# Kernel tuning notes

Hardware: AMD Instinct MI355X
Metric: run time of the kernel (lower is better)

Reference implementation:

```python
import jax, jax.numpy as jnp
import numpy as np
from jax import lax

# NOTE: ResidualConvBlock and SS2DChanelFirst are reconstructed from the repo's
# conventions: ResidualConvBlock = act(conv3x3 -> act -> conv3x3 + 1x1 skip);
# SS2DChanelFirst = standard VMamba SS2D (in_proj -> dw-conv3x3 -> SiLU ->
# 4-direction cross-scan selective scan -> cross-merge -> LayerNorm -> *SiLU(z)
# gate -> out_proj) operating on NCHW tensors.

B, CIN, H, W = 4, 6, 64, 64
DM, DI, K, N, R, NL, GROUPS = 72, 144, 4, 8, 4, 2, 12


def conv2d(x, w, b=None, groups=1):
    out = lax.conv_general_dilated(x, w, (1, 1), 'SAME',
                                   dimension_numbers=('NCHW', 'OIHW', 'NCHW'),
                                   feature_group_count=groups)
    if b is not None:
        out = out + b[None, :, None, None]
    return out


def lrelu(x, s):
    return jnp.where(x >= 0, x, s * x)


def selective_scan(u, delta, A, Bs, Cs, D):
    # u, delta: (b,K,C,L); A: (K,C,N); Bs, Cs: (b,K,N,L); D: (K,C)
    b, k, c, l = u.shape
    n = A.shape[-1]
    ul = jnp.moveaxis(u, -1, 0)
    dl = jnp.moveaxis(delta, -1, 0)
    Bl = jnp.moveaxis(Bs, -1, 0)
    Cl = jnp.moveaxis(Cs, -1, 0)
    h0 = jnp.zeros((b, k, c, n), u.dtype)

    def step(h, xt):
        d_t, u_t, B_t, C_t = xt
        h = h * jnp.exp(d_t[..., None] * A) + (d_t * u_t)[..., None] * B_t[:, :, None, :]
        return h, jnp.einsum('bkcn,bkn->bkc', h, C_t)

    _, ys = lax.scan(step, h0, (dl, ul, Bl, Cl))
    return jnp.moveaxis(ys, 0, -1) + u * D[None, :, :, None]


def ss2d(x, in_w, dw_w, dw_b, xp_w, dtp_w, dtp_b, A_logs, Ds, ong, onb, op_w):
    b, dm, h_, w_ = x.shape
    l = h_ * w_
    xz = jnp.einsum('ec,bchw->behw', in_w, x)  # (b, 2*DI, h, w)
    xi, z = xz[:, :DI], xz[:, DI:]
    xi = jax.nn.silu(conv2d(xi, dw_w, dw_b, groups=DI))
    # cross-scan: row-major, col-major, and their reverses
    x0 = xi.reshape(b, DI, l)
    x1 = jnp.swapaxes(xi, 2, 3).reshape(b, DI, l)
    xs = jnp.stack([x0, x1, x0[..., ::-1], x1[..., ::-1]], axis=1)  # (b,4,DI,l)
    x_dbl = jnp.einsum('bkdl,kcd->bkcl', xs, xp_w)  # (b,4,R+2N,l)
    dts, Bs, Cs = x_dbl[:, :, :R], x_dbl[:, :, R:R + N], x_dbl[:, :, R + N:]
    dts = jnp.einsum('bkrl,kdr->bkdl', dts, dtp_w)
    delta = jax.nn.softplus(dts + dtp_b[None, :, :, None])
    A = -jnp.exp(A_logs).reshape(K, DI, N)
    ys = selective_scan(xs, delta, A, Bs, Cs, Ds.reshape(K, DI))  # (b,4,DI,l)
    # cross-merge
    y = ys[:, 0] + ys[:, 2, :, ::-1]
    yt = ys[:, 1] + ys[:, 3, :, ::-1]
    y = y + jnp.swapaxes(yt.reshape(b, DI, w_, h_), 2, 3).reshape(b, DI, l)
    y = jnp.swapaxes(y, 1, 2)  # (b,l,DI)
    mu = y.mean(-1, keepdims=True)
    var = ((y - mu) ** 2).mean(-1, keepdims=True)
    y = (y - mu) / jnp.sqrt(var + 1e-5) * ong + onb
    y = y * jax.nn.silu(jnp.swapaxes(z.reshape(b, DI, l), 1, 2))
    out = jnp.einsum('bld,ed->ble', y, op_w)  # (b,l,DM)
    return jnp.swapaxes(out, 1, 2).reshape(b, dm, h_, w_)


def groupnorm(x, g, bta, groups):
    b, c, h_, w_ = x.shape
    xg = x.reshape(b, groups, c // groups, h_ * w_)
    mu = xg.mean((2, 3), keepdims=True)
    var = ((xg - mu) ** 2).mean((2, 3), keepdims=True)
    xg = (xg - mu) / jnp.sqrt(var + 1e-5)
    return xg.reshape(b, c, h_, w_) * g[None, :, None, None] + bta[None, :, None, None]


def setup_inputs() -> dict:
    key = jax.random.key(0)
    ks = iter(jax.random.split(key, 32))
    nrm = lambda shp, s=0.05: jax.random.normal(next(ks), shp, jnp.float32) * s
    inp = {
        'image': jax.random.normal(next(ks), (B, CIN, H, W), jnp.float32),
        'cb_w1': nrm((DM, CIN, 3, 3), 0.1), 'cb_b1': nrm((DM,), 0.02),
        'cb_w2': nrm((DM, DM, 3, 3), 0.05), 'cb_b2': nrm((DM,), 0.02),
        'cb_ws': nrm((DM, CIN, 1, 1), 0.1), 'cb_bs': nrm((DM,), 0.02),
        'in_w': nrm((NL, 2 * DI, DM), 0.05),
        'dw_w': nrm((NL, DI, 1, 3, 3), 0.1), 'dw_b': nrm((NL, DI), 0.02),
        'xp_w': nrm((NL, K, R + 2 * N, DI), 0.05),
        'dtp_w': nrm((NL, K, DI, R), 0.1), 'dtp_b': nrm((NL, K, DI), 0.1),
        'A_logs': nrm((NL, K * DI, N), 0.5),
        'Ds': jnp.ones((NL, K * DI), jnp.float32) + nrm((NL, K * DI), 0.05),
        'ong': jnp.ones((NL, DI), jnp.float32), 'onb': jnp.zeros((NL, DI), jnp.float32),
        'op_w': nrm((NL, DM, DI), 0.05),
        'gn_g': jnp.ones((NL, DM), jnp.float32), 'gn_b': jnp.zeros((NL, DM), jnp.float32),
        'l1_w': nrm((NL, DM, DM), 0.1), 'l1_b': nrm((NL, DM), 0.02),
        'l2_w': nrm((NL, DM, DM), 0.1), 'l2_b': nrm((NL, DM), 0.02),
        'shrink_w': nrm((CIN, DM, 3, 3), 0.05), 'shrink_b': nrm((CIN,), 0.02),
    }
    return inp


def reference(image, cb_w1, cb_b1, cb_w2, cb_b2, cb_ws, cb_bs, in_w, dw_w, dw_b,
              xp_w, dtp_w, dtp_b, A_logs, Ds, ong, onb, op_w, gn_g, gn_b,
              l1_w, l1_b, l2_w, l2_b, shrink_w, shrink_b):
    # ResidualConvBlock (expand 6 -> 72), leaky_relu
    h = lrelu(conv2d(image, cb_w1, cb_b1), 0.01)
    h = conv2d(h, cb_w2, cb_b2) + conv2d(image, cb_ws, cb_bs)
    x = lrelu(h, 0.01)
    for i in range(NL):
        x = ss2d(x, in_w[i], dw_w[i], dw_b[i], xp_w[i], dtp_w[i], dtp_b[i],
                 A_logs[i], Ds[i], ong[i], onb[i], op_w[i])
        x = groupnorm(x, gn_g[i], gn_b[i], GROUPS)
        x = jnp.einsum('oc,bchw->bohw', l1_w[i], x) + l1_b[i][None, :, None, None]
        x = lrelu(x, 0.04)
        x = jnp.einsum('oc,bchw->bohw', l2_w[i], x) + l2_b[i][None, :, None, None]
    x = conv2d(x, shrink_w, shrink_b)
    return jax.nn.sigmoid(x)
```

## Files before the change

### kernel.cpp

```cpp
#include <hip/hip_runtime.h>
#include <math.h>

#define BB 4
#define CI 6
#define LL 4096
#define DMC 72
#define DIC 144
#define KD 4
#define NS 8
#define RD 4
#define NLAYER 2
#define GRP 12
#define NCH 256
#define TS 16
#define SP 72
#define PPN (66*SP)
#define L2E 1.4426950408889634f

__device__ __forceinline__ float sigmoidf_(float x){ return 1.f/(1.f+__expf(-x)); }
__device__ __forceinline__ float siluf_(float x){ return x*sigmoidf_(x); }
__device__ __forceinline__ float softplusf_(float x){
  return fmaxf(x,0.f) + __logf(1.f + __expf(-fabsf(x)));
}

__device__ __forceinline__ int padidx(int p){ return SP*(p>>6) + (p&63) + SP + 4; }

#define LOAD9(ip, a) do { \
  a[0]=(ip)[-SP-1]; a[1]=(ip)[-SP]; a[2]=(ip)[-SP+1]; \
  a[3]=(ip)[-1];    a[4]=(ip)[0];   a[5]=(ip)[1];     \
  a[6]=(ip)[SP-1];  a[7]=(ip)[SP];  a[8]=(ip)[SP+1];  } while(0)

__device__ __forceinline__ void load6(const float* __restrict__ base, float v[6]){
  v[0] = base[-1];
  float4 f = *(const float4*)base;
  v[1]=f.x; v[2]=f.y; v[3]=f.z; v[4]=f.w;
  v[5] = base[4];
}

__global__ void k_halo(float* __restrict__ pads, int nplanes){
  int plane = blockIdx.x;
  if (plane >= nplanes) return;
  int t = threadIdx.x;
  if (t >= 260) return;
  float* pl = pads + (size_t)plane*PPN;
  int row, col;
  if (t < 132){
    row = (t < 66) ? 0 : 65;
    col = 3 + (t % 66);
  } else {
    int j = t - 132;
    col = (j < 64) ? 3 : 68;
    row = 1 + (j & 63);
  }
  pl[row*SP + col] = 0.f;
}

__global__ void k_pad_img(const float* __restrict__ img, float* __restrict__ img_pad){
  int idx = blockIdx.x*256 + threadIdx.x;
  if (idx >= BB*CI*LL) return;
  int p = idx & 4095; int bc = idx >> 12;
  img_pad[(size_t)bc*PPN + padidx(p)] = img[idx];
}

__global__ void k_conv1(const float* __restrict__ img_pad, const float* __restrict__ w,
                        const float* __restrict__ bias, float* __restrict__ tmp_pad){
  int bid = blockIdx.x;
  int tile = bid & 3; int r = bid >> 2; int o = r % DMC; int b = r / DMC;
  int p0 = tile*1024 + threadIdx.x*4;
  int pb = padidx(p0);
  float bv = bias[o];
  float acc[4] = {bv,bv,bv,bv};
  #pragma unroll
  for (int ic=0; ic<CI; ++ic){
    const float* ip = img_pad + (size_t)(b*CI+ic)*PPN + pb;
    const float* wr = w + (o*CI+ic)*9;
    #pragma unroll
    for (int rr=0; rr<3; ++rr){
      float v[6]; load6(ip + (rr-1)*SP, v);
      float w0=wr[rr*3], w1=wr[rr*3+1], w2v=wr[rr*3+2];
      #pragma unroll
      for (int q=0;q<4;++q) acc[q] += v[q]*w0 + v[q+1]*w1 + v[q+2]*w2v;
    }
  }
  #pragma unroll
  for (int q=0;q<4;++q) acc[q] = acc[q] >= 0.f ? acc[q] : 0.01f*acc[q];
  *(float4*)(tmp_pad + (size_t)(b*DMC+o)*PPN + pb) = make_float4(acc[0],acc[1],acc[2],acc[3]);
}

__global__ void k_conv2init(const float* __restrict__ img, const float* __restrict__ b2,
                            const float* __restrict__ wsc, const float* __restrict__ bsc,
                            float* __restrict__ xout){
  int bid = blockIdx.x;
  int t = bid & 15; int r = bid >> 4; int og = r % 18; int b = r / 18;
  int p = t*256 + threadIdx.x;
  float acc[4];
  #pragma unroll
  for (int j=0;j<4;++j) acc[j] = b2[og*4+j] + bsc[og*4+j];
  #pragma unroll
  for (int ic=0; ic<CI; ++ic){
    float v = img[((b*CI+ic)<<12)+p];
    #pragma unroll
    for (int j=0;j<4;++j) acc[j] += v * wsc[(og*4+j)*CI+ic];
  }
  #pragma unroll
  for (int j=0;j<4;++j)
    xout[((b*DMC+og*4+j)<<12)+p] = acc[j];
}

__global__ void k_conv2(const float* __restrict__ tmp_pad,
                        const float* __restrict__ w2, float* __restrict__ xout){
  int bid = blockIdx.x;
  int t = bid & 15; int r = bid >> 4; int og = r % 18; r /= 18;
  int icg = r & 1; int b = r >> 1;
  int p = t*256 + threadIdx.x;
  int pb = padidx(p);
  float acc[4] = {0.f,0.f,0.f,0.f};
  const float* ipb = tmp_pad + (size_t)b*DMC*PPN + pb;
  const float* wb  = w2 + (size_t)(og*4)*DMC*9;
  #pragma unroll 2
  for (int ii=0; ii<36; ++ii){
    int ic = icg*36 + ii;
    const float* ip = ipb + (size_t)ic*PPN;
    float a[9]; LOAD9(ip, a);
    const float* wp = wb + ic*9;
    #pragma unroll
    for (int j=0;j<4;++j){
      float s = 0.f;
      #pragma unroll
      for (int q=0;q<9;++q) s += a[q]*wp[(size_t)j*DMC*9 + q];
      acc[j] += s;
    }
  }
  #pragma unroll
  for (int j=0;j<4;++j)
    atomicAdd(xout + ((b*DMC+og*4+j)<<12)+p, acc[j]);
}

__global__ void k_xz(const float* __restrict__ x, const float* __restrict__ inw,
                     float* __restrict__ xz_pad, float* __restrict__ z_t, int relu){
  int bid = blockIdx.x;
  int t = bid & 15; int r = bid >> 4; int eg = r % 36; int b = r / 36;
  int p = t*256 + threadIdx.x;
  float acc[8] = {0.f,0.f,0.f,0.f,0.f,0.f,0.f,0.f};
  for (int c0=0; c0<DMC; c0+=4){
    float a[4];
    #pragma unroll
    for (int q=0;q<4;++q) a[q] = x[((b*DMC+c0+q)<<12)+p];
    if (relu){
      #pragma unroll
      for (int q=0;q<4;++q) a[q] = a[q] >= 0.f ? a[q] : 0.01f*a[q];
    }
    #pragma unroll
    for (int j=0;j<8;++j){
      float4 w = *(const float4*)(inw + (eg*8+j)*DMC + c0);
      acc[j] += a[0]*w.x + a[1]*w.y + a[2]*w.z + a[3]*w.w;
    }
  }
  if (eg < 18){
    int pb = padidx(p);
    #pragma unroll
    for (int j=0;j<8;++j) xz_pad[(size_t)(b*DIC+eg*8+j)*PPN + pb] = acc[j];
  } else {
    float* zb = z_t + ((size_t)b*LL+p)*DIC + (eg*8-DIC);
    *(float4*)(zb)   = make_float4(acc[0],acc[1],acc[2],acc[3]);
    *(float4*)(zb+4) = make_float4(acc[4],acc[5],acc[6],acc[7]);
  }
}

__global__ void k_dw(const float* __restrict__ xz_pad, const float* __restrict__ dww,
                     const float* __restrict__ dwb, float* __restrict__ xi_t){
  int bid = blockIdx.x;
  int tile = bid & 3; int r = bid >> 2; int c = r % DIC; int b = r / DIC;
  int p0 = tile*1024 + threadIdx.x*4;
  int pb = padidx(p0);
  const float* ip = xz_pad + (size_t)(b*DIC+c)*PPN + pb;
  const float* wp = dww + c*9;
  float bv = dwb[c];
  float acc[4] = {bv,bv,bv,bv};
  #pragma unroll
  for (int rr=0; rr<3; ++rr){
    float v[6]; load6(ip + (rr-1)*SP, v);
    float w0=wp[rr*3], w1=wp[rr*3+1], w2v=wp[rr*3+2];
    #pragma unroll
    for (int q=0;q<4;++q) acc[q] += v[q]*w0 + v[q+1]*w1 + v[q+2]*w2v;
  }
  #pragma unroll
  for (int q=0;q<4;++q)
    xi_t[((size_t)b*LL+p0+q)*DIC + c] = siluf_(acc[q]);
}

__global__ void k_xdbl(const float* __restrict__ xi_t, const float* __restrict__ xpw,
                       float* __restrict__ xdbl){
  int bid = blockIdx.x;
  int t = bid & 15; int r = bid >> 4;
  int kk = r & 3; r >>= 2; int part = r & 3; int b = r >> 2;
  int p = t*256 + threadIdx.x;
  const float* xib = xi_t + ((size_t)b*LL + p)*DIC;
  const float* wk = xpw + (size_t)(kk*20 + part*5)*DIC;
  float acc[5] = {0.f,0.f,0.f,0.f,0.f};
  for (int d=0; d<DIC; d+=4){
    float4 v = *(const float4*)(xib + d);
    #pragma unroll
    for (int c=0;c<5;++c){
      float4 w = *(const float4*)(wk + (size_t)c*DIC + d);
      acc[c] += v.x*w.x + v.y*w.y + v.z*w.z + v.w*w.w;
    }
  }
  float* dst = xdbl + ((size_t)(b*KD+kk)*LL + p)*20 + part*5;
  #pragma unroll
  for (int c=0;c<5;++c) dst[c] = acc[c];
}

__device__ __forceinline__ void scan_decode(int idx, int& b, int& k, int& ch, int& c){
  c = idx % DIC;
  int r = idx / DIC;
  ch = r % NCH;
  r /= NCH;
  k = r & 3; b = r >> 2;
}

__device__ __forceinline__ void scan_affine(int k, int ch, int& ps0, int& sk){
  int l0 = ch*TS;
  if (k == 0){ ps0 = l0; sk = 1; }
  else if (k == 1){ ps0 = ((l0 & 63) << 6) | (l0 >> 6); sk = 64; }
  else if (k == 2){ ps0 = (LL-1) - l0; sk = -1; }
  else { int m0 = (LL-1) - l0; ps0 = ((m0 & 63) << 6) | (m0 >> 6); sk = -64; }
}

__global__ void k_p1(const float* __restrict__ xi_t, const float* __restrict__ xdbl,
                     const float* __restrict__ dtpw, const float* __restrict__ dtpb,
                     const float* __restrict__ alog,
                     float* __restrict__ cumA, float* __restrict__ hp){
  int idx = blockIdx.x*256 + threadIdx.x;
  if (idx >= BB*KD*NCH*DIC) return;
  int b,k,ch,c; scan_decode(idx,b,k,ch,c);
  float Arow[NS];
  #pragma unroll
  for (int n=0;n<NS;++n) Arow[n] = -__expf(alog[(k*DIC+c)*NS+n]) * L2E;
  float4 wdt = *(const float4*)(dtpw + (k*DIC+c)*RD);
  float bdt = dtpb[k*DIC+c];
  int ps0, sk; scan_affine(k, ch, ps0, sk);
  const float* row = xdbl + (size_t)(b*KD+k)*LL*20 + (size_t)ps0*20;
  const float* up  = xi_t + (size_t)b*LL*DIC + c + (size_t)ps0*DIC;
  long rstep = (long)sk*20;
  long ustep = (long)sk*DIC;
  float h[NS];
  #pragma unroll
  for (int n=0;n<NS;++n) h[n]=0.f;
  float sumd = 0.f;
  #pragma unroll 4
  for (int t=0; t<TS; ++t){
    float4 q0 = *(const float4*)(row);
    float4 q1 = *(const float4*)(row+4);
    float4 q2 = *(const float4*)(row+8);
    float u = *up;
    float dt = bdt + q0.x*wdt.x + q0.y*wdt.y + q0.z*wdt.z + q0.w*wdt.w;
    dt = softplusf_(dt);
    sumd += dt;
    float du = dt*u;
    float Bv[NS] = {q1.x,q1.y,q1.z,q1.w,q2.x,q2.y,q2.z,q2.w};
    #pragma unroll
    for (int n=0;n<NS;++n)
      h[n] = h[n]*exp2f(dt*Arow[n]) + du*Bv[n];
    row += rstep; up += ustep;
  }
  size_t base = ((size_t)((b*KD+k)*NCH + ch)*NS)*DIC + c;
  #pragma unroll
  for (int n=0;n<NS;++n) hp[base + n*DIC] = h[n];
  #pragma unroll
  for (int n=0;n<NS;++n) cumA[base + n*DIC] = exp2f(sumd*Arow[n]);
}

__global__ void k_p2(float* __restrict__ cumA, float* __restrict__ hp,
                     float* __restrict__ gnstats){
  if (blockIdx.x == 0 && threadIdx.x < 2*BB*GRP) gnstats[threadIdx.x] = 0.f;
  int idx = blockIdx.x*256 + threadIdx.x;
  if (idx >= BB*KD*NS*DIC) return;
  int c = idx % DIC; int n = (idx/DIC) % NS; int bk = idx/(DIC*NS);
  float h = 0.f;
  #pragma unroll 8
  for (int ch=0; ch<NCH; ++ch){
    size_t base = ((size_t)(bk*NCH+ch)*NS + n)*DIC + c;
    float a = cumA[base];
    float pp = hp[base];
    cumA[base] = 0.f;
    hp[base] = h;
    h = a*h + pp;
  }
}

__global__ void k_p3(const float* __restrict__ xi_t, const float* __restrict__ xdbl,
                     const float* __restrict__ dtpw, const float* __restrict__ dtpb,
                     const float* __restrict__ alog, const float* __restrict__ Dsv,
                     const float* __restrict__ hin, float* __restrict__ y_t){
  int idx = blockIdx.x*256 + threadIdx.x;
  if (idx >= BB*KD*NCH*DIC) return;
  int b,k,ch,c; scan_decode(idx,b,k,ch,c);
  float Arow[NS];
  #pragma unroll
  for (int n=0;n<NS;++n) Arow[n] = -__expf(alog[(k*DIC+c)*NS+n]) * L2E;
  float4 wdt = *(const float4*)(dtpw + (k*DIC+c)*RD);
  float bdt = dtpb[k*DIC+c];
  float Dv = Dsv[k*DIC+c];
  int ps0, sk; scan_affine(k, ch, ps0, sk);
  const float* row = xdbl + (size_t)(b*KD+k)*LL*20 + (size_t)ps0*20;
  const float* up  = xi_t + (size_t)b*LL*DIC + c + (size_t)ps0*DIC;
  float* yp        = y_t  + (size_t)b*LL*DIC + c + (size_t)ps0*DIC;
  long rstep = (long)sk*20;
  long ustep = (long)sk*DIC;
  float h[NS];
  size_t base = ((size_t)((b*KD+k)*NCH + ch)*NS)*DIC + c;
  #pragma unroll
  for (int n=0;n<NS;++n) h[n] = hin[base + n*DIC];
  #pragma unroll 4
  for (int t=0; t<TS; ++t){
    float4 q0 = *(const float4*)(row);
    float4 q1 = *(const float4*)(row+4);
    float4 q2 = *(const float4*)(row+8);
    float4 q3 = *(const float4*)(row+12);
    float4 q4 = *(const float4*)(row+16);
    float u = *up;
    float dt = bdt + q0.x*wdt.x + q0.y*wdt.y + q0.z*wdt.z + q0.w*wdt.w;
    dt = softplusf_(dt);
    float du = dt*u;
    float Bv[NS] = {q1.x,q1.y,q1.z,q1.w,q2.x,q2.y,q2.z,q2.w};
    float Cv[NS] = {q3.x,q3.y,q3.z,q3.w,q4.x,q4.y,q4.z,q4.w};
    float y = 0.f;
    #pragma unroll
    for (int n=0;n<NS;++n){
      h[n] = h[n]*exp2f(dt*Arow[n]) + du*Bv[n];
      y += h[n]*Cv[n];
    }
    y += u*Dv;
    atomicAdd(yp, y);
    row += rstep; up += ustep; yp += ustep;
  }
}

__global__ void k_lnz(float* __restrict__ y_t, const float* __restrict__ z_t,
                      const float* __restrict__ ong, const float* __restrict__ onb){
  int gid = blockIdx.x*256 + threadIdx.x;
  int wid = gid >> 6;
  int lane = gid & 63;
  if (wid >= BB*LL) return;
  size_t rb = (size_t)wid * DIC;
  float v0 = y_t[rb + lane];
  float v1 = y_t[rb + 64 + lane];
  float v2 = (lane < 16) ? y_t[rb + 128 + lane] : 0.f;
  float s = v0 + v1 + v2;
  float q = v0*v0 + v1*v1 + v2*v2;
  #pragma unroll
  for (int o=32; o>0; o>>=1){ s += __shfl_xor(s,o,64); q += __shfl_xor(q,o,64); }
  float mu = s*(1.f/DIC);
  float var = q*(1.f/DIC) - mu*mu;
  float rs = rsqrtf(var + 1e-5f);
  float z0 = z_t[rb + lane];
  y_t[rb + lane] = ((v0-mu)*rs*ong[lane] + onb[lane]) * siluf_(z0);
  float z1 = z_t[rb + 64 + lane];
  y_t[rb + 64 + lane] = ((v1-mu)*rs*ong[64+lane] + onb[64+lane]) * siluf_(z1);
  if (lane < 16){
    float z2 = z_t[rb + 128 + lane];
    y_t[rb + 128 + lane] = ((v2-mu)*rs*ong[128+lane] + onb[128+lane]) * siluf_(z2);
  }
}

__global__ void k_oproj(const float* __restrict__ yn, const float* __restrict__ opw,
                        float* __restrict__ xout, float* __restrict__ gnstats){
  int bid = blockIdx.x;
  int t = bid & 15; int r = bid >> 4; int og = r % 18; int b = r / 18;
  int p = t*256 + threadIdx.x;
  const float* yb = yn + ((size_t)b*LL + p)*DIC;
  float acc[4] = {0.f,0.f,0.f,0.f};
  for (int d=0; d<DIC; d+=4){
    float4 v = *(const float4*)(yb + d);
    #pragma unroll
    for (int j=0;j<4;++j){
      float4 w = *(const float4*)(opw + (og*4+j)*DIC + d);
      acc[j] += v.x*w.x + v.y*w.y + v.z*w.z + v.w*w.w;
    }
  }
  #pragma unroll
  for (int j=0;j<4;++j)
    xout[((size_t)(b*DMC+og*4+j)<<12)+p] = acc[j];
  int c0 = og*4;
  int gA = c0/6;
  int nA = 6 - (c0 - gA*6);
  float sA=0.f,qA=0.f,sB=0.f,qB=0.f;
  #pragma unroll
  for (int j=0;j<4;++j){
    float v = acc[j];
    if (j < nA){ sA += v; qA += v*v; } else { sB += v; qB += v*v; }
  }
  #pragma unroll
  for (int o=32; o>0; o>>=1){
    sA += __shfl_xor(sA,o,64); qA += __shfl_xor(qA,o,64);
    sB += __shfl_xor(sB,o,64); qB += __shfl_xor(qB,o,64);
  }
  if ((threadIdx.x & 63) == 0){
    atomicAdd(gnstats + (b*GRP+gA)*2,     sA);
    atomicAdd(gnstats + (b*GRP+gA)*2 + 1, qA);
    if (nA < 4){
      atomicAdd(gnstats + (b*GRP+gA+1)*2,     sB);
      atomicAdd(gnstats + (b*GRP+gA+1)*2 + 1, qB);
    }
  }
}

__global__ void k_dense1(const float* __restrict__ xin, const float* __restrict__ gnstats,
                         const float* __restrict__ gng, const float* __restrict__ gnb,
                         const float* __restrict__ w, const float* __restrict__ bias,
                         float* __restrict__ xout){
  __shared__ float As[DMC], Bs[DMC];
  int bid = blockIdx.x;
  int t = bid & 15; int r = bid >> 4; int eg = r % 18; int b = r / 18;
  if (threadIdx.x < DMC){
    int c = threadIdx.x; int gr = c/6;
    float s = gnstats[(b*GRP+gr)*2];
    float q = gnstats[(b*GRP+gr)*2 + 1];
    const float inv = 1.f/(6.f*LL);
    float mu = s*inv;
    float var = q*inv - mu*mu;
    float rs = rsqrtf(var + 1e-5f);
    float A = rs*gng[c];
    As[c] = A;
    Bs[c] = gnb[c] - mu*A;
  }
  __syncthreads();
  int p = t*256 + threadIdx.x;
  float acc[4];
  #pragma unroll
  for (int j=0;j<4;++j) acc[j] = bias[eg*4+j];
  for (int c0=0; c0<DMC; c0+=4){
    float a[4];
    #pragma unroll
    for (int q=0;q<4;++q){
      float v = xin[((size_t)(b*DMC+c0+q)<<12)+p];
      a[q] = v*As[c0+q] + Bs[c0+q];
    }
    #pragma unroll
    for (int j=0;j<4;++j){
      float4 w0 = *(const float4*)(w + (eg*4+j)*DMC + c0);
      acc[j] += a[0]*w0.x + a[1]*w0.y + a[2]*w0.z + a[3]*w0.w;
    }
  }
  #pragma unroll
  for (int j=0;j<4;++j)
    xout[((size_t)(b*DMC+eg*4+j)<<12)+p] = acc[j];
}

__global__ void k_dense2(const float* __restrict__ xin, const float* __restrict__ w,
                         const float* __restrict__ bias, float* __restrict__ xout,
                         float* __restrict__ pad_out){
  int bid = blockIdx.x;
  int t = bid & 15; int r = bid >> 4; int eg = r % 18; int b = r / 18;
  int p = t*256 + threadIdx.x;
  float acc[4];
  #pragma unroll
  for (int j=0;j<4;++j) acc[j] = bias[eg*4+j];
  for (int c0=0; c0<DMC; c0+=4){
    float a[4];
    #pragma unroll
    for (int q=0;q<4;++q){
      float v = xin[((size_t)(b*DMC+c0+q)<<12)+p];
      a[q] = v >= 0.f ? v : 0.04f*v;
    }
    #pragma unroll
    for (int j=0;j<4;++j){
      float4 w0 = *(const float4*)(w + (eg*4+j)*DMC + c0);
      acc[j] += a[0]*w0.x + a[1]*w0.y + a[2]*w0.z + a[3]*w0.w;
    }
  }
  int pb = padidx(p);
  #pragma unroll
  for (int j=0;j<4;++j){
    xout[((size_t)(b*DMC+eg*4+j)<<12)+p] = acc[j];
    if (pad_out) pad_out[(size_t)(b*DMC+eg*4+j)*PPN + pb] = acc[j];
  }
}

__global__ void k_shrinkA(const float* __restrict__ x_pad, const float* __restrict__ w,
                          float* __restrict__ pacc){
  int bid = blockIdx.x;
  int t = bid & 15; int r = bid >> 4; int icg = r % 24; int b = r / 24;
  int p = t*256 + threadIdx.x;
  int pb = padidx(p);
  float acc[6] = {0.f,0.f,0.f,0.f,0.f,0.f};
  const float* ipb = x_pad + (size_t)b*DMC*PPN + pb;
  #pragma unroll
  for (int ii=0; ii<3; ++ii){
    int ic = icg*3 + ii;
    const float* ip = ipb + (size_t)ic*PPN;
    float a[9]; LOAD9(ip, a);
    #pragma unroll
    for (int o=0;o<6;++o){
      const float* wp = w + (o*DMC+ic)*9;
      float s = 0.f;
      #pragma unroll
      for (int q=0;q<9;++q) s += a[q]*wp[q];
      acc[o] += s;
    }
  }
  #pragma unroll
  for (int o=0;o<6;++o)
    atomicAdd(pacc + ((size_t)(b*CI+o)<<12)+p, acc[o]);
}

__global__ void k_sig(const float* __restrict__ pacc, const float* __restrict__ bias,
                      float* __restrict__ out){
  int idx = blockIdx.x*256 + threadIdx.x;
  if (idx >= BB*CI*LL) return;
  int o = (idx>>12) % CI;
  out[idx] = sigmoidf_(pacc[idx] + bias[o]);
}

extern "C" void kernel_launch(void* const* d_in, const int* in_sizes, int n_in,
                              void* d_out, int out_size, void* d_ws, size_t ws_size,
                              hipStream_t stream){
  const float* image = (const float*)d_in[0];
  const float* cb_w1 = (const float*)d_in[1];
  const float* cb_b1 = (const float*)d_in[2];
  const float* cb_w2 = (const float*)d_in[3];
  const float* cb_b2 = (const float*)d_in[4];
  const float* cb_ws = (const float*)d_in[5];
  const float* cb_bs = (const float*)d_in[6];
  const float* in_w  = (const float*)d_in[7];
  const float* dw_w  = (const float*)d_in[8];
  const float* dw_b  = (const float*)d_in[9];
  const float* xp_w  = (const float*)d_in[10];
  const float* dtp_w = (const float*)d_in[11];
  const float* dtp_b = (const float*)d_in[12];
  const float* A_logs= (const float*)d_in[13];
  const float* Ds    = (const float*)d_in[14];
  const float* ong   = (const float*)d_in[15];
  const float* onb   = (const float*)d_in[16];
  const float* op_w  = (const float*)d_in[17];
  const float* gn_g  = (const float*)d_in[18];
  const float* gn_b  = (const float*)d_in[19];
  const float* l1_w  = (const float*)d_in[20];
  const float* l1_b  = (const float*)d_in[21];
  const float* l2_w  = (const float*)d_in[22];
  const float* l2_b  = (const float*)d_in[23];
  const float* sh_w  = (const float*)d_in[24];
  const float* sh_b  = (const float*)d_in[25];

  const size_t SZ_X  = (size_t)BB*DMC*LL;
  const size_t SZ_C  = (size_t)BB*DIC*LL;
  const size_t SZ_XD = (size_t)BB*KD*20*LL;
  const size_t SZ_HP = (size_t)BB*KD*NCH*NS*DIC;
  const size_t SZ_IP = (size_t)BB*CI*PPN;
  const size_t SZ_TP = (size_t)BB*DMC*PPN;
  const size_t SZ_ZP = (size_t)BB*DIC*PPN;

  float* ws = (float*)d_ws;
  size_t off = 0;
  float* x     = ws + off; off += SZ_X;
  float* tmp   = ws + off; off += SZ_X;
  float* z_t   = ws + off; off += SZ_C;
  float* xi_t  = ws + off; off += SZ_C;
  float* xdbl  = ws + off; off += SZ_XD;
  float* cumA  = ws + off; off += SZ_HP;
  float* hp    = ws + off; off += SZ_HP;
  float* pads  = ws + off;
  float* img_pad = pads;
  float* tmp_pad = img_pad + SZ_IP;
  float* xz_pad  = tmp_pad + SZ_TP;
  off += SZ_IP + SZ_TP + SZ_ZP;
  float* gnstats = ws + off; off += 2*BB*GRP;
  if (ws_size < off*sizeof(float)) return;
  float* y_t = cumA;

  dim3 blk(256);
  const int NPLANES = BB*CI + BB*DMC + BB*DIC;

  k_halo<<<dim3(NPLANES), blk, 0, stream>>>(pads, NPLANES);
  k_pad_img<<<dim3(BB*CI*16), blk, 0, stream>>>(image, img_pad);
  k_conv1<<<dim3(BB*DMC*4), blk, 0, stream>>>(img_pad, cb_w1, cb_b1, tmp_pad);
  k_conv2init<<<dim3(BB*18*16), blk, 0, stream>>>(image, cb_b2, cb_ws, cb_bs, x);
  k_conv2<<<dim3(BB*2*18*16), blk, 0, stream>>>(tmp_pad, cb_w2, x);

  for (int i=0; i<NLAYER; ++i){
    const float* in_w_i  = in_w  + (size_t)i*2*DIC*DMC;
    const float* dw_w_i  = dw_w  + (size_t)i*DIC*9;
    const float* dw_b_i  = dw_b  + (size_t)i*DIC;
    const float* xp_w_i  = xp_w  + (size_t)i*KD*20*DIC;
    const float* dtp_w_i = dtp_w + (size_t)i*KD*DIC*RD;
    const float* dtp_b_i = dtp_b + (size_t)i*KD*DIC;
    const float* alog_i  = A_logs+ (size_t)i*KD*DIC*NS;
    const float* Ds_i    = Ds    + (size_t)i*KD*DIC;
    const float* ong_i   = ong   + (size_t)i*DIC;
    const float* onb_i   = onb   + (size_t)i*DIC;
    const float* op_w_i  = op_w  + (size_t)i*DMC*DIC;
    const float* gn_g_i  = gn_g  + (size_t)i*DMC;
    const float* gn_b_i  = gn_b  + (size_t)i*DMC;
    const float* l1_w_i  = l1_w  + (size_t)i*DMC*DMC;
    const float* l1_b_i  = l1_b  + (size_t)i*DMC;
    const float* l2_w_i  = l2_w  + (size_t)i*DMC*DMC;
    const float* l2_b_i  = l2_b  + (size_t)i*DMC;

    k_xz  <<<dim3(BB*36*16), blk, 0, stream>>>(x, in_w_i, xz_pad, z_t, (i==0)?1:0);
    k_dw  <<<dim3(BB*DIC*4), blk, 0, stream>>>(xz_pad, dw_w_i, dw_b_i, xi_t);
    k_xdbl<<<dim3(BB*4*KD*16), blk, 0, stream>>>(xi_t, xp_w_i, xdbl);
    k_p1  <<<dim3(BB*KD*NCH*DIC/256), blk, 0, stream>>>(xi_t, xdbl, dtp_w_i, dtp_b_i, alog_i, cumA, hp);
    k_p2  <<<dim3(BB*KD*NS*DIC/256), blk, 0, stream>>>(cumA, hp, gnstats);
    k_p3  <<<dim3(BB*KD*NCH*DIC/256), blk, 0, stream>>>(xi_t, xdbl, dtp_w_i, dtp_b_i, alog_i, Ds_i, hp, y_t);
    k_lnz <<<dim3(BB*LL/4), blk, 0, stream>>>(y_t, z_t, ong_i, onb_i);
    k_oproj<<<dim3(BB*18*16), blk, 0, stream>>>(y_t, op_w_i, x, gnstats);
    k_dense1<<<dim3(BB*18*16), blk, 0, stream>>>(x, gnstats, gn_g_i, gn_b_i, l1_w_i, l1_b_i, tmp);
    k_dense2<<<dim3(BB*18*16), blk, 0, stream>>>(tmp, l2_w_i, l2_b_i, x,
                                                 (i==NLAYER-1) ? tmp_pad : (float*)nullptr);
  }

  hipMemsetAsync(tmp, 0, (size_t)BB*CI*LL*sizeof(float), stream);
  k_shrinkA<<<dim3(BB*24*16), blk, 0, stream>>>(tmp_pad, sh_w, tmp);
  k_sig<<<dim3((BB*CI*LL+255)/256), blk, 0, stream>>>(tmp, sh_b, (float*)d_out);
}
```

Baseline: 592.7 us.

## Tile out-projection through shared memory and split GroupNorm stats into own kernel

The out-projection now stages a 64-pixel by 72-channel slice of the normalized activations transposed in shared memory, and each wave computes 9 output channels. Each block handles half of the input channels and adds its partial sums into the output with atomics, so the LayerNorm kernel now zeroes the output buffer first. GroupNorm statistics move out of the projection into a separate reduction kernel that rereads the output. The aim is to reuse each activation load across more outputs and raise per-thread work, at the cost of global atomics, one extra kernel launch, and an extra pass over the output.

```diff
diff --git a/kernel.cpp b/kernel.cpp
--- a/kernel.cpp
+++ b/kernel.cpp
@@ -338,8 +338,11 @@
 }
 
 __global__ void k_lnz(float* __restrict__ y_t, const float* __restrict__ z_t,
-                      const float* __restrict__ ong, const float* __restrict__ onb){
+                      const float* __restrict__ ong, const float* __restrict__ onb,
+                      float* __restrict__ xzero){
   int gid = blockIdx.x*256 + threadIdx.x;
+  xzero[gid] = 0.f;
+  if (gid < (int)(BB*DMC*LL - BB*LL*64)) xzero[gid + BB*LL*64] = 0.f;
   int wid = gid >> 6;
   int lane = gid & 63;
   if (wid >= BB*LL) return;
@@ -365,44 +368,55 @@
 }
 
 __global__ void k_oproj(const float* __restrict__ yn, const float* __restrict__ opw,
-                        float* __restrict__ xout, float* __restrict__ gnstats){
-  int bid = blockIdx.x;
-  int t = bid & 15; int r = bid >> 4; int og = r % 18; int b = r / 18;
-  int p = t*256 + threadIdx.x;
-  const float* yb = yn + ((size_t)b*LL + p)*DIC;
-  float acc[4] = {0.f,0.f,0.f,0.f};
-  for (int d=0; d<DIC; d+=4){
-    float4 v = *(const float4*)(yb + d);
-    #pragma unroll
-    for (int j=0;j<4;++j){
-      float4 w = *(const float4*)(opw + (og*4+j)*DIC + d);
-      acc[j] += v.x*w.x + v.y*w.y + v.z*w.z + v.w*w.w;
-    }
-  }
-  #pragma unroll
-  for (int j=0;j<4;++j)
-    xout[((size_t)(b*DMC+og*4+j)<<12)+p] = acc[j];
-  int c0 = og*4;
-  int gA = c0/6;
-  int nA = 6 - (c0 - gA*6);
-  float sA=0.f,qA=0.f,sB=0.f,qB=0.f;
-  #pragma unroll
-  for (int j=0;j<4;++j){
-    float v = acc[j];
-    if (j < nA){ sA += v; qA += v*v; } else { sB += v; qB += v*v; }
-  }
-  #pragma unroll
-  for (int o=32; o>0; o>>=1){
-    sA += __shfl_xor(sA,o,64); qA += __shfl_xor(qA,o,64);
-    sB += __shfl_xor(sB,o,64); qB += __shfl_xor(qB,o,64);
-  }
-  if ((threadIdx.x & 63) == 0){
-    atomicAdd(gnstats + (b*GRP+gA)*2,     sA);
-    atomicAdd(gnstats + (b*GRP+gA)*2 + 1, qA);
-    if (nA < 4){
-      atomicAdd(gnstats + (b*GRP+gA+1)*2,     sB);
-      atomicAdd(gnstats + (b*GRP+gA+1)*2 + 1, qB);
-    }
+                        float* __restrict__ xout){
+  __shared__ float ly[72*65];
+  int bid = blockIdx.x;
+  int dhalf = bid & 1; int r = bid >> 1;
+  int tile = r & 63; int b = r >> 6;
+  int pstart = tile*64;
+  const float* src = yn + ((size_t)b*LL + pstart)*DIC + dhalf*72;
+  for (int i = threadIdx.x; i < 64*72; i += 512){
+    int px = i / 72; int d = i - px*72;
+    ly[d*65 + px] = src[(size_t)px*DIC + d];
+  }
+  __syncthreads();
+  int px = threadIdx.x & 63;
+  int ocg = __builtin_amdgcn_readfirstlane(threadIdx.x >> 6);
+  float acc[9];
+  #pragma unroll
+  for (int j=0;j<9;++j) acc[j]=0.f;
+  const float* wb = opw + (size_t)ocg*9*DIC + dhalf*72;
+  #pragma unroll 4
+  for (int d=0; d<72; ++d){
+    float a = ly[d*65 + px];
+    #pragma unroll
+    for (int j=0;j<9;++j) acc[j] += a * wb[(size_t)j*DIC + d];
+  }
+  #pragma unroll
+  for (int j=0;j<9;++j)
+    atomicAdd(xout + ((size_t)(b*DMC + ocg*9 + j)<<12) + pstart + px, acc[j]);
+}
+
+__global__ void k_gnA(const float* __restrict__ x, float* __restrict__ stats){
+  __shared__ float s1[256], s2[256];
+  int bid = blockIdx.x;
+  int t = bid & 15; int r = bid >> 4; int gr = r % GRP; int b = r / GRP;
+  float ls=0.f, lq=0.f;
+  #pragma unroll
+  for (int it=0; it<6; ++it){
+    int i = t*1536 + it*256 + threadIdx.x;
+    int c = gr*6 + (i>>12); int p = i & 4095;
+    float v = x[((size_t)(b*DMC+c)<<12)+p];
+    ls += v; lq += v*v;
+  }
+  s1[threadIdx.x]=ls; s2[threadIdx.x]=lq; __syncthreads();
+  for (int s=128; s>0; s>>=1){
+    if (threadIdx.x < s){ s1[threadIdx.x]+=s1[threadIdx.x+s]; s2[threadIdx.x]+=s2[threadIdx.x+s]; }
+    __syncthreads();
+  }
+  if (threadIdx.x == 0){
+    atomicAdd(stats + (b*GRP+gr)*2,     s1[0]);
+    atomicAdd(stats + (b*GRP+gr)*2 + 1, s2[0]);
   }
 }
 
@@ -603,8 +617,9 @@
     k_p1  <<<dim3(BB*KD*NCH*DIC/256), blk, 0, stream>>>(xi_t, xdbl, dtp_w_i, dtp_b_i, alog_i, cumA, hp);
     k_p2  <<<dim3(BB*KD*NS*DIC/256), blk, 0, stream>>>(cumA, hp, gnstats);
     k_p3  <<<dim3(BB*KD*NCH*DIC/256), blk, 0, stream>>>(xi_t, xdbl, dtp_w_i, dtp_b_i, alog_i, Ds_i, hp, y_t);
-    k_lnz <<<dim3(BB*LL/4), blk, 0, stream>>>(y_t, z_t, ong_i, onb_i);
-    k_oproj<<<dim3(BB*18*16), blk, 0, stream>>>(y_t, op_w_i, x, gnstats);
+    k_lnz <<<dim3(BB*LL/4), blk, 0, stream>>>(y_t, z_t, ong_i, onb_i, x);
+    k_oproj<<<dim3(BB*64*2), dim3(512), 0, stream>>>(y_t, op_w_i, x);
+    k_gnA <<<dim3(BB*GRP*16), blk, 0, stream>>>(x, gnstats);
     k_dense1<<<dim3(BB*18*16), blk, 0, stream>>>(x, gnstats, gn_g_i, gn_b_i, l1_w_i, l1_b_i, tmp);
     k_dense2<<<dim3(BB*18*16), blk, 0, stream>>>(tmp, l2_w_i, l2_b_i, x,
                                                  (i==NLAYER-1) ? tmp_pad : (float*)nullptr);
```

New measurement: 498.1 us. 1.19x faster.
